# Optimization experiments

Hardware: AMD Instinct MI355X
Metric: run time of the kernel (lower is better)

Reference implementation:

```python
import jax, jax.numpy as jnp
import numpy as np

B, N, F = 64, 512, 30          # batch, pf candidates, raw features
NDIM0, NDIM = 2, 4             # coord dims: layer0 uses 2, rest use n_dim_gnn=4
NOUT, NLAYERS = 64, 5          # GNN layer width / count
NDENSE = 128
BN_EPS = 1e-3                  # keras BatchNormalization default epsilon


def setup_inputs() -> dict:
    key = jax.random.key(0)
    ks = jax.random.split(key, 20)
    xx = jax.random.normal(ks[0], (B, N, F), jnp.float32)
    # validity mask: first L_b candidates valid
    lengths = jax.random.randint(ks[1], (B,), N // 4, N + 1)
    valid = (jnp.arange(N)[None, :] < lengths[:, None]).astype(jnp.float32)
    pt = jax.random.randint(ks[2], (B, N), 0, 8).astype(jnp.float32)
    pvq = jax.random.randint(ks[3], (B, N), 0, 8).astype(jnp.float32)
    fpv = jax.random.randint(ks[4], (B, N), 0, 4).astype(jnp.float32)
    xx = xx.at[:, :, 0].set(valid).at[:, :, 27].set(pt).at[:, :, 28].set(pvq).at[:, :, 29].set(fpv)
    g = lambda k, s, sc=0.05: jax.random.normal(k, s, jnp.float32) * sc
    d_in0 = 33  # 2+2+2 embeddings + 27 float features
    return {
        "xx": xx,
        "emb1": g(ks[5], (8, 2), 0.5),
        "emb2": g(ks[6], (8, 2), 0.5),
        "emb3": g(ks[7], (4, 2), 0.5),
        "A0": g(ks[8], ((d_in0 + 1) * 2 - 1, NOUT)),   # [67,64]
        "b0": g(ks[9], (NOUT,)),
        "A_rest": g(ks[10], (NLAYERS - 1, (NOUT + 1) * 2 - 1, NOUT)),  # [4,129,64]
        "b_rest": g(ks[11], (NLAYERS - 1, NOUT)),
        "bn_gamma": jnp.ones((NLAYERS, NOUT), jnp.float32),
        "bn_beta": jnp.zeros((NLAYERS, NOUT), jnp.float32),
        "dW0": g(ks[12], (N * NOUT, NDENSE), 0.01),
        "db0": g(ks[13], (NDENSE,)),
        "dW1": g(ks[14], (NDENSE, NDENSE)),
        "db1": g(ks[15], (NDENSE,)),
        "dbn_gamma": jnp.ones((2, NDENSE), jnp.float32),
        "dbn_beta": jnp.zeros((2, NDENSE), jnp.float32),
        "W2": g(ks[16], (NDENSE, 2)),
        "b2": g(ks[17], (2,)),
    }


def _bn(x, g, b):
    # inference BatchNorm with moving_mean=0, moving_var=1 (initial stats)
    return g * x * (1.0 / jnp.sqrt(1.0 + BN_EPS)) + b


def _gnn_layer(x, mask, n_dim, A, b):
    # x: [B,N,Fin], mask: [B,N]. Original builds [B,N,N,Fin+1] via tile/reshape;
    # algebraically the reduction over senders i factorizes:
    #   ss_feat[b,j] = x[b,j] * mask[b,j] * sum_i exp(-10*d_ij)
    #   ss_last[b,j] = mask[b,j] * sum_i d_ij * exp(-10*d_ij)
    c = x[..., -n_dim:]
    diff = c[:, :, None, :] - c[:, None, :, :]      # [B,N,N,n_dim]
    dist = jnp.sum(diff * diff, axis=-1)            # [B,N,N] squared distance
    w = jnp.exp(-10.0 * dist)
    S = jnp.sum(w, axis=1)                          # [B,N] per receiver j
    T = jnp.sum(dist * w, axis=1)                   # [B,N]
    ss_feat = x * (mask * S)[..., None] - x         # subtract concat(x, 0)
    ss_last = (mask * T)[..., None]
    xcat = jnp.concatenate([x, ss_feat, ss_last], axis=-1)  # [B,N,2*Fin+1]
    return (xcat @ A + b) * mask[..., None]


def _forward(xx, emb1, emb2, emb3, A0, b0, A_rest, b_rest, bn_gamma, bn_beta,
             dW0, db0, dW1, db1, dbn_gamma, dbn_beta, W2, b2):
    mask = xx[:, :, 0]
    e1 = emb1[jnp.abs(xx[:, :, 27]).astype(jnp.int32)]
    e2 = emb2[jnp.abs(xx[:, :, 28]).astype(jnp.int32)]
    e3 = emb3[jnp.abs(xx[:, :, 29]).astype(jnp.int32)]
    x = jnp.concatenate([e1, e2, e3, xx[:, :, :27]], axis=-1)  # [B,N,33]
    x = jnp.tanh(_bn(_gnn_layer(x, mask, NDIM0, A0, b0), bn_gamma[0], bn_beta[0]))
    for k in range(NLAYERS - 1):
        x = _gnn_layer(x, mask, NDIM, A_rest[k], b_rest[k])
        x = jnp.tanh(_bn(x, bn_gamma[k + 1], bn_beta[k + 1]))
    x = x.reshape(B, N * NOUT)
    x = jax.nn.sigmoid(_bn(x @ dW0 + db0, dbn_gamma[0], dbn_beta[0]))
    x = jax.nn.sigmoid(_bn(x @ dW1 + db1, dbn_gamma[1], dbn_beta[1]))
    x = x @ W2 + b2                                  # [B,2]
    # mode == 'dm': concat zeros on the right
    return jnp.concatenate([x, jnp.zeros((B, 2), x.dtype)], axis=1)


def reference(xx, emb1, emb2, emb3, A0, b0, A_rest, b_rest, bn_gamma, bn_beta,
              dW0, db0, dW1, db1, dbn_gamma, dbn_beta, W2, b2):
    return _forward(xx, emb1, emb2, emb3, A0, b0, A_rest, b_rest, bn_gamma, bn_beta,
                    dW0, db0, dW1, db1, dbn_gamma, dbn_beta, W2, b2)
```

## Files before the change

### kernel.cpp

```cpp
#include <hip/hip_runtime.h>
#include <math.h>

#define B_ 64
#define N_ 512
#define R_ (B_*N_)
#define INV_S 0.9995003746877732f

__device__ __forceinline__ float fast_tanh(float y){
  return 1.f - 2.f*__builtin_amdgcn_rcpf(1.f + __expf(2.f*y));
}
__device__ __forceinline__ float fast_sigmoid(float v){
  return __builtin_amdgcn_rcpf(1.f + __expf(-v));
}

struct GnnArgs {
  const float* xx;
  const float* emb1; const float* emb2; const float* emb3;
  const float* A0;  const float* b0;
  const float* Ar;  const float* br;
  const float* bng; const float* bnb;
  float4* cb0; float4* cb1;
  unsigned int* bar;
  float* xfinal;
};

__global__ __launch_bounds__(512, 4) void gnn_fused(GnnArgs g)
{
  __shared__ float alo[64*64];
  __shared__ float ahi[64*64];
  __shared__ float xs[64*68];
  __shared__ float4 cl[512];
  __shared__ float spart[512], tpart[512];
  __shared__ float scl[64], tcl[64], ml[64];

  const int tid   = threadIdx.x;
  const int b     = blockIdx.x;
  const int jc    = blockIdx.y;
  const int jloc  = jc*64;
  const int rbase = b*N_;
  const int cg = tid & 15, rg = tid >> 4;
  const int o0 = cg*4,  lr0 = rg*2;
  unsigned int* barp = g.bar + b*32;

  for (int k = 0; k < 5; ++k){
    const float* A;  const float* bi;  int K, KP;
    if (k == 0){ A = g.A0;                        bi = g.b0;            K = 33; KP = 36; }
    else       { A = g.Ar + (size_t)(k-1)*129*64; bi = g.br + (k-1)*64; K = 64; KP = 64; }
    const float* gam = g.bng + k*64;
    const float* bet = g.bnb + k*64;

    if (k == 0){
      for (int idx = tid; idx < 36*64; idx += 512){
        int f = idx >> 6;
        alo[idx] = (f < 33) ? A[idx] : 0.f;
        ahi[idx] = (f < 33) ? A[33*64 + idx] : 0.f;
      }
      {
        const float* xr = g.xx + (size_t)(rbase + tid)*30;
        cl[tid] = make_float4(xr[25], xr[26], 0.f, 0.f);
      }
      if (tid < 64){
        const float* row = g.xx + (size_t)(rbase + jloc + tid)*30;
        float v[30];
#pragma unroll
        for (int i=0;i<30;i++) v[i] = row[i];
        int i1 = (int)fabsf(v[27]);
        int i2 = (int)fabsf(v[28]);
        int i3 = (int)fabsf(v[29]);
        float* o = &xs[tid*68];
        o[0]=g.emb1[i1*2+0]; o[1]=g.emb1[i1*2+1];
        o[2]=g.emb2[i2*2+0]; o[3]=g.emb2[i2*2+1];
        o[4]=g.emb3[i3*2+0]; o[5]=g.emb3[i3*2+1];
#pragma unroll
        for (int i=0;i<27;i++) o[6+i] = v[i];
        o[33]=0.f; o[34]=0.f; o[35]=0.f;
        ml[tid] = v[0];
      }
    } else {
      __syncthreads();
      if (tid == 0){
        __builtin_amdgcn_fence(__ATOMIC_RELEASE, "agent");
        __hip_atomic_fetch_add(barp, 1u, __ATOMIC_RELAXED, __HIP_MEMORY_SCOPE_AGENT);
      }
      {
        const float4* A4 = (const float4*)A;
        float4* alo4 = (float4*)alo;
        float4* ahi4 = (float4*)ahi;
        for (int idx = tid; idx < 1024; idx += 512){
          alo4[idx] = A4[idx];
          ahi4[idx] = A4[1024 + idx];
        }
      }
      if (tid == 0){
        unsigned int tgt = 8u*(unsigned int)k;
        while (__hip_atomic_load(barp, __ATOMIC_RELAXED, __HIP_MEMORY_SCOPE_AGENT) < tgt)
          __builtin_amdgcn_s_sleep(2);
        __builtin_amdgcn_fence(__ATOMIC_ACQUIRE, "agent");
      }
      __syncthreads();
      const float4* cbr = ((k & 1) ? g.cb0 : g.cb1) + rbase;
      cl[tid] = cbr[tid];
    }
    __syncthreads();

    {
      int jj = tid & 63, ic = tid >> 6, base = ic*64;
      float4 cj = cl[jloc + jj];
      float Ss = 0.f, Ts = 0.f;
#pragma unroll 8
      for (int i=0;i<64;i++){
        float4 ci = cl[base+i];
        float d0 = cj.x-ci.x, d1 = cj.y-ci.y, d2 = cj.z-ci.z, d3 = cj.w-ci.w;
        float dist = d0*d0 + d1*d1 + d2*d2 + d3*d3;
        float w = __expf(-10.f*dist);
        Ss += w; Ts += dist*w;
      }
      spart[tid] = Ss;
      tpart[tid] = Ts;
    }
    __syncthreads();

    if (tid < 64){
      float S = 0.f, T = 0.f;
#pragma unroll
      for (int c=0;c<8;c++){
        S += spart[tid + 64*c];
        T += tpart[tid + 64*c];
      }
      float m = ml[tid];
      scl[tid] = m*S - 1.f;
      tcl[tid] = m*T;
    }
    __syncthreads();

    float4 acc1[2], acc2[2];
#pragma unroll
    for (int rr=0;rr<2;rr++){
      acc1[rr] = make_float4(0.f,0.f,0.f,0.f);
      acc2[rr] = make_float4(0.f,0.f,0.f,0.f);
    }
#pragma unroll 2
    for (int kc = 0; kc < KP; kc += 4){
      float4 a1[4], a2[4], xv[2];
#pragma unroll
      for (int uu=0;uu<4;uu++){
        a1[uu] = *(const float4*)&alo[(kc+uu)*64 + o0];
        a2[uu] = *(const float4*)&ahi[(kc+uu)*64 + o0];
      }
#pragma unroll
      for (int rr=0;rr<2;rr++)
        xv[rr] = *(const float4*)&xs[(lr0+rr)*68 + kc];
#pragma unroll
      for (int uu=0;uu<4;uu++){
#pragma unroll
        for (int rr=0;rr<2;rr++){
          float xu = ((const float*)&xv[rr])[uu];
          acc1[rr].x = fmaf(xu, a1[uu].x, acc1[rr].x);
          acc1[rr].y = fmaf(xu, a1[uu].y, acc1[rr].y);
          acc1[rr].z = fmaf(xu, a1[uu].z, acc1[rr].z);
          acc1[rr].w = fmaf(xu, a1[uu].w, acc1[rr].w);
          acc2[rr].x = fmaf(xu, a2[uu].x, acc2[rr].x);
          acc2[rr].y = fmaf(xu, a2[uu].y, acc2[rr].y);
          acc2[rr].z = fmaf(xu, a2[uu].z, acc2[rr].z);
          acc2[rr].w = fmaf(xu, a2[uu].w, acc2[rr].w);
        }
      }
    }
    __syncthreads();

    float4 alast = *(const float4*)&A[(size_t)2*K*64 + o0];
    float4 bo = *(const float4*)&bi[o0];
    float4 go = *(const float4*)&gam[o0];
    float4 bb = *(const float4*)&bet[o0];
    float4* cbw = (k & 1) ? g.cb1 : g.cb0;
#pragma unroll
    for (int rr=0;rr<2;rr++){
      int lr = lr0 + rr;
      float sc = scl[lr], tc = tcl[lr], m = ml[lr];
      float4 v;
      v.x = (acc1[rr].x + sc*acc2[rr].x + tc*alast.x + bo.x)*m;
      v.y = (acc1[rr].y + sc*acc2[rr].y + tc*alast.y + bo.y)*m;
      v.z = (acc1[rr].z + sc*acc2[rr].z + tc*alast.z + bo.z)*m;
      v.w = (acc1[rr].w + sc*acc2[rr].w + tc*alast.w + bo.w)*m;
      float4 t;
      t.x = fast_tanh(go.x*(v.x*INV_S) + bb.x);
      t.y = fast_tanh(go.y*(v.y*INV_S) + bb.y);
      t.z = fast_tanh(go.z*(v.z*INV_S) + bb.z);
      t.w = fast_tanh(go.w*(v.w*INV_S) + bb.w);
      if (k < 4){
        *(float4*)&xs[lr*68 + o0] = t;
        if (cg == 15) cbw[rbase + jloc + lr] = t;
      } else {
        *(float4*)&g.xfinal[(size_t)(rbase + jloc + lr)*64 + o0] = t;
      }
    }
  }
}

__global__ __launch_bounds__(256) void dense0_partial(
    const float* __restrict__ X, const float* __restrict__ W,
    float* __restrict__ partial)
{
  __shared__ float xt[64*32];
  __shared__ float wt[32*128];
  int tid = threadIdx.x;
  int k0 = blockIdx.x*128;
  int og = (tid & 15)*8;
  int rg = (tid >> 4)*4;
  float acc[4][8];
#pragma unroll
  for (int a=0;a<4;a++)
#pragma unroll
    for (int u=0;u<8;u++) acc[a][u]=0.f;
  for (int kt = 0; kt < 128; kt += 32){
    __syncthreads();
    for (int idx = tid; idx < 512; idx += 256){
      int r = idx >> 3, kq = idx & 7;
      *(float4*)&xt[r*32 + kq*4] =
          *(const float4*)&X[(size_t)r*32768 + k0 + kt + kq*4];
    }
    {
      const float4* Wc = (const float4*)&W[(size_t)(k0+kt)*128];
      float4* wt4 = (float4*)wt;
      for (int idx = tid; idx < 1024; idx += 256) wt4[idx] = Wc[idx];
    }
    __syncthreads();
#pragma unroll 4
    for (int k=0;k<32;k++){
      float4 w0 = *(const float4*)&wt[k*128 + og];
      float4 w1 = *(const float4*)&wt[k*128 + og + 4];
      float xs[4];
#pragma unroll
      for (int rr=0;rr<4;rr++) xs[rr] = xt[(rg+rr)*32 + k];
#pragma unroll
      for (int rr=0;rr<4;rr++){
        acc[rr][0] = fmaf(xs[rr], w0.x, acc[rr][0]);
        acc[rr][1] = fmaf(xs[rr], w0.y, acc[rr][1]);
        acc[rr][2] = fmaf(xs[rr], w0.z, acc[rr][2]);
        acc[rr][3] = fmaf(xs[rr], w0.w, acc[rr][3]);
        acc[rr][4] = fmaf(xs[rr], w1.x, acc[rr][4]);
        acc[rr][5] = fmaf(xs[rr], w1.y, acc[rr][5]);
        acc[rr][6] = fmaf(xs[rr], w1.z, acc[rr][6]);
        acc[rr][7] = fmaf(xs[rr], w1.w, acc[rr][7]);
      }
    }
  }
  float* pb = partial + (size_t)blockIdx.x*8192;
#pragma unroll
  for (int rr=0;rr<4;rr++){
    *(float4*)&pb[(rg+rr)*128 + og]     = *(float4*)&acc[rr][0];
    *(float4*)&pb[(rg+rr)*128 + og + 4] = *(float4*)&acc[rr][4];
  }
}

__global__ __launch_bounds__(256) void dense_head(
    const float* __restrict__ partial,
    const float* __restrict__ db0, const float* __restrict__ dg0,
    const float* __restrict__ dbb0,
    const float* __restrict__ dW1, const float* __restrict__ db1,
    const float* __restrict__ dg1, const float* __restrict__ dbb1,
    const float* __restrict__ W2, const float* __restrict__ b2,
    float* __restrict__ out)
{
  __shared__ float sred[256];
  __shared__ float h[128];
  __shared__ float red0[128], red1[128];
  int tid = threadIdx.x;
  int b = blockIdx.x;
  int o = tid & 127, ph = tid >> 7;
  float s = 0.f;
#pragma unroll 16
  for (int p = ph*128; p < ph*128+128; p++)
    s += partial[(size_t)p*8192 + b*128 + o];
  sred[tid] = s;
  __syncthreads();
  if (tid < 128){
    float sum = sred[tid] + sred[tid+128];
    float v = dg0[tid]*((sum + db0[tid])*INV_S) + dbb0[tid];
    h[tid] = fast_sigmoid(v);
  }
  __syncthreads();
  if (tid < 128){
    float acc = 0.f;
#pragma unroll 8
    for (int k=0;k<128;k++) acc = fmaf(h[k], dW1[k*128 + tid], acc);
    float v = dg1[tid]*((acc + db1[tid])*INV_S) + dbb1[tid];
    float h1 = fast_sigmoid(v);
    red0[tid] = h1 * W2[tid*2+0];
    red1[tid] = h1 * W2[tid*2+1];
  }
  __syncthreads();
  for (int st=64; st>0; st>>=1){
    if (tid < st){ red0[tid] += red0[tid+st]; red1[tid] += red1[tid+st]; }
    __syncthreads();
  }
  if (tid == 0){
    out[b*4+0] = red0[0] + b2[0];
    out[b*4+1] = red1[0] + b2[1];
    out[b*4+2] = 0.f;
    out[b*4+3] = 0.f;
  }
}

extern "C" void kernel_launch(void* const* d_in, const int* in_sizes, int n_in,
                              void* d_out, int out_size, void* d_ws, size_t ws_size,
                              hipStream_t stream)
{
  const float* xx   = (const float*)d_in[0];
  const float* emb1 = (const float*)d_in[1];
  const float* emb2 = (const float*)d_in[2];
  const float* emb3 = (const float*)d_in[3];
  const float* A0   = (const float*)d_in[4];
  const float* b0   = (const float*)d_in[5];
  const float* Ar   = (const float*)d_in[6];
  const float* br   = (const float*)d_in[7];
  const float* bng  = (const float*)d_in[8];
  const float* bnb  = (const float*)d_in[9];
  const float* dW0  = (const float*)d_in[10];
  const float* db0  = (const float*)d_in[11];
  const float* dW1  = (const float*)d_in[12];
  const float* db1  = (const float*)d_in[13];
  const float* dbg  = (const float*)d_in[14];
  const float* dbb  = (const float*)d_in[15];
  const float* W2   = (const float*)d_in[16];
  const float* b2   = (const float*)d_in[17];

  float* ws = (float*)d_ws;
  float*  xA      = ws;
  float*  partial = xA + (size_t)R_*64;
  float4* cb0     = (float4*)(partial + (size_t)256*8192);
  float4* cb1     = cb0 + R_;
  unsigned int* bar = (unsigned int*)(cb1 + R_);

  hipMemsetAsync(bar, 0, 64*32*sizeof(unsigned int), stream);

  GnnArgs ga;
  ga.xx = xx; ga.emb1 = emb1; ga.emb2 = emb2; ga.emb3 = emb3;
  ga.A0 = A0; ga.b0 = b0; ga.Ar = Ar; ga.br = br;
  ga.bng = bng; ga.bnb = bnb;
  ga.cb0 = cb0; ga.cb1 = cb1; ga.bar = bar; ga.xfinal = xA;

  hipLaunchKernelGGL(gnn_fused, dim3(64,8), dim3(512), 0, stream, ga);

  dense0_partial<<<256, 256, 0, stream>>>(xA, dW0, partial);
  dense_head<<<B_, 256, 0, stream>>>(partial, db0, dbg, dbb,
                                     dW1, db1, dbg + 128, dbb + 128,
                                     W2, b2, (float*)d_out);
}
```

Before: 219.1 us.

## Overlap per-layer GEMM with inter-block barrier wait and fold coord reduction

```diff
diff --git a/kernel.cpp b/kernel.cpp
--- a/kernel.cpp
+++ b/kernel.cpp
@@ -24,6 +24,47 @@
   float* xfinal;
 };
 
+template<int KP>
+__device__ __forceinline__ void gemm_tile(const float* __restrict__ alo,
+                                          const float* __restrict__ ahi,
+                                          const float* __restrict__ xsrc,
+                                          int o0, int lr0,
+                                          float4 acc1[2], float4 acc2[2])
+{
+#pragma unroll
+  for (int rr=0;rr<2;rr++){
+    acc1[rr] = make_float4(0.f,0.f,0.f,0.f);
+    acc2[rr] = make_float4(0.f,0.f,0.f,0.f);
+  }
+#pragma unroll 2
+  for (int kc = 0; kc < KP; kc += 4){
+    float4 a1[4], a2[4], xv[2];
+#pragma unroll
+    for (int uu=0;uu<4;uu++){
+      a1[uu] = *(const float4*)&alo[(kc+uu)*64 + o0];
+      a2[uu] = *(const float4*)&ahi[(kc+uu)*64 + o0];
+    }
+#pragma unroll
+    for (int rr=0;rr<2;rr++)
+      xv[rr] = *(const float4*)&xsrc[(lr0+rr)*68 + kc];
+#pragma unroll
+    for (int uu=0;uu<4;uu++){
+#pragma unroll
+      for (int rr=0;rr<2;rr++){
+        float xu = ((const float*)&xv[rr])[uu];
+        acc1[rr].x = fmaf(xu, a1[uu].x, acc1[rr].x);
+        acc1[rr].y = fmaf(xu, a1[uu].y, acc1[rr].y);
+        acc1[rr].z = fmaf(xu, a1[uu].z, acc1[rr].z);
+        acc1[rr].w = fmaf(xu, a1[uu].w, acc1[rr].w);
+        acc2[rr].x = fmaf(xu, a2[uu].x, acc2[rr].x);
+        acc2[rr].y = fmaf(xu, a2[uu].y, acc2[rr].y);
+        acc2[rr].z = fmaf(xu, a2[uu].z, acc2[rr].z);
+        acc2[rr].w = fmaf(xu, a2[uu].w, acc2[rr].w);
+      }
+    }
+  }
+}
+
 __global__ __launch_bounds__(512, 4) void gnn_fused(GnnArgs g)
 {
   __shared__ float alo[64*64];
@@ -31,7 +72,7 @@
   __shared__ float xs[64*68];
   __shared__ float4 cl[512];
   __shared__ float spart[512], tpart[512];
-  __shared__ float scl[64], tcl[64], ml[64];
+  __shared__ float ml[64];
 
   const int tid   = threadIdx.x;
   const int b     = blockIdx.x;
@@ -43,9 +84,9 @@
   unsigned int* barp = g.bar + b*32;
 
   for (int k = 0; k < 5; ++k){
-    const float* A;  const float* bi;  int K, KP;
-    if (k == 0){ A = g.A0;                        bi = g.b0;            K = 33; KP = 36; }
-    else       { A = g.Ar + (size_t)(k-1)*129*64; bi = g.br + (k-1)*64; K = 64; KP = 64; }
+    const float* A;  const float* bi;  int K;
+    if (k == 0){ A = g.A0;                        bi = g.b0;            K = 33; }
+    else       { A = g.Ar + (size_t)(k-1)*129*64; bi = g.br + (k-1)*64; K = 64; }
     const float* gam = g.bng + k*64;
     const float* bet = g.bnb + k*64;
 
@@ -91,6 +132,19 @@
           ahi4[idx] = A4[1024 + idx];
         }
       }
+    }
+    __syncthreads();
+
+    float4 acc1[2], acc2[2];
+    if (k == 0) gemm_tile<36>(alo, ahi, xs, o0, lr0, acc1, acc2);
+    else        gemm_tile<64>(alo, ahi, xs, o0, lr0, acc1, acc2);
+
+    float4 alast = *(const float4*)&A[(size_t)2*K*64 + o0];
+    float4 bo = *(const float4*)&bi[o0];
+    float4 go = *(const float4*)&gam[o0];
+    float4 bb = *(const float4*)&bet[o0];
+
+    if (k >= 1){
       if (tid == 0){
         unsigned int tgt = 8u*(unsigned int)k;
         while (__hip_atomic_load(barp, __ATOMIC_RELAXED, __HIP_MEMORY_SCOPE_AGENT) < tgt)
@@ -100,83 +154,51 @@
       __syncthreads();
       const float4* cbr = ((k & 1) ? g.cb0 : g.cb1) + rbase;
       cl[tid] = cbr[tid];
-    }
-    __syncthreads();
+      __syncthreads();
+    }
 
     {
       int jj = tid & 63, ic = tid >> 6, base = ic*64;
-      float4 cj = cl[jloc + jj];
       float Ss = 0.f, Ts = 0.f;
+      if (k == 0){
+        float4 cj = cl[jloc + jj];
 #pragma unroll 8
-      for (int i=0;i<64;i++){
-        float4 ci = cl[base+i];
-        float d0 = cj.x-ci.x, d1 = cj.y-ci.y, d2 = cj.z-ci.z, d3 = cj.w-ci.w;
-        float dist = d0*d0 + d1*d1 + d2*d2 + d3*d3;
-        float w = __expf(-10.f*dist);
-        Ss += w; Ts += dist*w;
+        for (int i=0;i<64;i++){
+          float4 ci = cl[base+i];
+          float d0 = cj.x-ci.x, d1 = cj.y-ci.y;
+          float dist = d0*d0 + d1*d1;
+          float w = __expf(-10.f*dist);
+          Ss += w; Ts += dist*w;
+        }
+      } else {
+        float4 cj = cl[jloc + jj];
+#pragma unroll 8
+        for (int i=0;i<64;i++){
+          float4 ci = cl[base+i];
+          float d0 = cj.x-ci.x, d1 = cj.y-ci.y, d2 = cj.z-ci.z, d3 = cj.w-ci.w;
+          float dist = d0*d0 + d1*d1 + d2*d2 + d3*d3;
+          float w = __expf(-10.f*dist);
+          Ss += w; Ts += dist*w;
+        }
       }
       spart[tid] = Ss;
       tpart[tid] = Ts;
     }
     __syncthreads();
 
-    if (tid < 64){
-      float S = 0.f, T = 0.f;
-#pragma unroll
-      for (int c=0;c<8;c++){
-        S += spart[tid + 64*c];
-        T += tpart[tid + 64*c];
-      }
-      float m = ml[tid];
-      scl[tid] = m*S - 1.f;
-      tcl[tid] = m*T;
-    }
-    __syncthreads();
-
-    float4 acc1[2], acc2[2];
-#pragma unroll
-    for (int rr=0;rr<2;rr++){
-      acc1[rr] = make_float4(0.f,0.f,0.f,0.f);
-      acc2[rr] = make_float4(0.f,0.f,0.f,0.f);
-    }
-#pragma unroll 2
-    for (int kc = 0; kc < KP; kc += 4){
-      float4 a1[4], a2[4], xv[2];
-#pragma unroll
-      for (int uu=0;uu<4;uu++){
-        a1[uu] = *(const float4*)&alo[(kc+uu)*64 + o0];
-        a2[uu] = *(const float4*)&ahi[(kc+uu)*64 + o0];
-      }
-#pragma unroll
-      for (int rr=0;rr<2;rr++)
-        xv[rr] = *(const float4*)&xs[(lr0+rr)*68 + kc];
-#pragma unroll
-      for (int uu=0;uu<4;uu++){
-#pragma unroll
-        for (int rr=0;rr<2;rr++){
-          float xu = ((const float*)&xv[rr])[uu];
-          acc1[rr].x = fmaf(xu, a1[uu].x, acc1[rr].x);
-          acc1[rr].y = fmaf(xu, a1[uu].y, acc1[rr].y);
-          acc1[rr].z = fmaf(xu, a1[uu].z, acc1[rr].z);
-          acc1[rr].w = fmaf(xu, a1[uu].w, acc1[rr].w);
-          acc2[rr].x = fmaf(xu, a2[uu].x, acc2[rr].x);
-          acc2[rr].y = fmaf(xu, a2[uu].y, acc2[rr].y);
-          acc2[rr].z = fmaf(xu, a2[uu].z, acc2[rr].z);
-          acc2[rr].w = fmaf(xu, a2[uu].w, acc2[rr].w);
-        }
-      }
-    }
-    __syncthreads();
-
-    float4 alast = *(const float4*)&A[(size_t)2*K*64 + o0];
-    float4 bo = *(const float4*)&bi[o0];
-    float4 go = *(const float4*)&gam[o0];
-    float4 bb = *(const float4*)&bet[o0];
     float4* cbw = (k & 1) ? g.cb1 : g.cb0;
 #pragma unroll
     for (int rr=0;rr<2;rr++){
       int lr = lr0 + rr;
-      float sc = scl[lr], tc = tcl[lr], m = ml[lr];
+      float S = 0.f, T = 0.f;
+#pragma unroll
+      for (int c=0;c<8;c++){
+        S += spart[lr + 64*c];
+        T += tpart[lr + 64*c];
+      }
+      float m = ml[lr];
+      float sc = m*S - 1.f;
+      float tc = m*T;
       float4 v;
       v.x = (acc1[rr].x + sc*acc2[rr].x + tc*alast.x + bo.x)*m;
       v.y = (acc1[rr].y + sc*acc2[rr].y + tc*alast.y + bo.y)*m;
@@ -229,19 +251,19 @@
     for (int k=0;k<32;k++){
       float4 w0 = *(const float4*)&wt[k*128 + og];
       float4 w1 = *(const float4*)&wt[k*128 + og + 4];
-      float xs[4];
-#pragma unroll
-      for (int rr=0;rr<4;rr++) xs[rr] = xt[(rg+rr)*32 + k];
+      float xv[4];
+#pragma unroll
+      for (int rr=0;rr<4;rr++) xv[rr] = xt[(rg+rr)*32 + k];
 #pragma unroll
       for (int rr=0;rr<4;rr++){
-        acc[rr][0] = fmaf(xs[rr], w0.x, acc[rr][0]);
-        acc[rr][1] = fmaf(xs[rr], w0.y, acc[rr][1]);
-        acc[rr][2] = fmaf(xs[rr], w0.z, acc[rr][2]);
-        acc[rr][3] = fmaf(xs[rr], w0.w, acc[rr][3]);
-        acc[rr][4] = fmaf(xs[rr], w1.x, acc[rr][4]);
-        acc[rr][5] = fmaf(xs[rr], w1.y, acc[rr][5]);
-        acc[rr][6] = fmaf(xs[rr], w1.z, acc[rr][6]);
-        acc[rr][7] = fmaf(xs[rr], w1.w, acc[rr][7]);
+        acc[rr][0] = fmaf(xv[rr], w0.x, acc[rr][0]);
+        acc[rr][1] = fmaf(xv[rr], w0.y, acc[rr][1]);
+        acc[rr][2] = fmaf(xv[rr], w0.z, acc[rr][2]);
+        acc[rr][3] = fmaf(xv[rr], w0.w, acc[rr][3]);
+        acc[rr][4] = fmaf(xv[rr], w1.x, acc[rr][4]);
+        acc[rr][5] = fmaf(xv[rr], w1.y, acc[rr][5]);
+        acc[rr][6] = fmaf(xv[rr], w1.z, acc[rr][6]);
+        acc[rr][7] = fmaf(xv[rr], w1.w, acc[rr][7]);
       }
     }
   }
```

Measured after the change: 226.8 us. 3.5% more time.
